# Kernel optimization log

Measured on AMD Instinct MI355X. Metric: run time of the kernel, lower is better.

## Reference

```python
import jax, jax.numpy as jnp
import numpy as np

D_MODEL = 1024
NUM_HEADS = 16
HEAD_DIM = D_MODEL // NUM_HEADS
B, S = 4, 2048


def _xavier(key, shape, gain=0.1):
    fan_in, fan_out = shape[1], shape[0]
    a = gain * np.sqrt(6.0 / (fan_in + fan_out))
    return jax.random.uniform(key, shape, jnp.float32, -a, a)


def setup_inputs() -> dict:
    key = jax.random.key(0)
    ks = jax.random.split(key, 11)
    inp = {
        "q": jax.random.normal(ks[0], (B, S, D_MODEL), jnp.float32),
        "k": jax.random.normal(ks[1], (B, S, D_MODEL), jnp.float32),
        "v": jax.random.normal(ks[2], (B, S, D_MODEL), jnp.float32),
        # nn.Linear weights are [out, in]; y = x @ W.T + b
        "Wq": _xavier(ks[3], (D_MODEL, D_MODEL)),
        "bq": jnp.zeros((D_MODEL,), jnp.float32),
        "Wk": _xavier(ks[4], (D_MODEL, D_MODEL)),
        "bk": jnp.zeros((D_MODEL,), jnp.float32),
        "Wv": _xavier(ks[5], (D_MODEL, D_MODEL)),
        "bv": jnp.zeros((D_MODEL,), jnp.float32),
        "Wo": _xavier(ks[6], (D_MODEL, D_MODEL)),
        "bo": jnp.zeros((D_MODEL,), jnp.float32),
    }
    return inp


def reference(q, k, v, Wq, bq, Wk, bk, Wv, bv, Wo, bo):
    b = q.shape[0]
    qh = (q @ Wq.T + bq).reshape(b, -1, NUM_HEADS, HEAD_DIM).transpose(0, 2, 1, 3)
    kh = (k @ Wk.T + bk).reshape(b, -1, NUM_HEADS, HEAD_DIM).transpose(0, 2, 1, 3)
    vh = (v @ Wv.T + bv).reshape(b, -1, NUM_HEADS, HEAD_DIM).transpose(0, 2, 1, 3)
    # NOTE: original (buggy) module scales by sqrt(d_model), not sqrt(head_dim)
    scale = 1.0 / jnp.sqrt(jnp.float32(D_MODEL))
    scores = jnp.einsum('bhqd,bhkd->bhqk', qh, kh) * scale  # [B,H,S,S]
    attn = jax.nn.softmax(scores, axis=-1)
    out = jnp.einsum('bhqk,bhkd->bhqd', attn, vh)
    out = out.transpose(0, 2, 1, 3).reshape(b, -1, D_MODEL)
    return out @ Wo.T + bo
```

## Files before the change

kernel.cpp:

```cpp
#include <hip/hip_runtime.h>

typedef unsigned short u16;
typedef short bf16x8 __attribute__((ext_vector_type(8)));
typedef float f32x4 __attribute__((ext_vector_type(4)));
typedef u16 u16x8 __attribute__((ext_vector_type(8)));

__device__ __forceinline__ u16 f2bf(float f) {
  unsigned u = __float_as_uint(f);
  u = u + 0x7fffu + ((u >> 16) & 1u);
  return (u16)(u >> 16);
}

__device__ __forceinline__ float fexp2(float x) {
#if __has_builtin(__builtin_amdgcn_exp2f)
  return __builtin_amdgcn_exp2f(x);
#else
  return exp2f(x);
#endif
}

#define GLD16(ldsp, gp)                                                         \
  __builtin_amdgcn_global_load_lds(                                             \
      (__attribute__((address_space(1))) void*)(void*)(gp),                     \
      (__attribute__((address_space(3))) void*)(ldsp), 16, 0, 0)

#define CVTPK(dst, lo, hi)                                                      \
  asm("v_cvt_pk_bf16_f32 %0, %1, %2" : "=v"(dst) : "v"(lo), "v"(hi))
#define PACK8(dst, a0, a1, a2, a3, a4, a5, a6, a7)                              \
  do {                                                                          \
    union { unsigned u_[4]; bf16x8 v_; } c_;                                    \
    CVTPK(c_.u_[0], a0, a1); CVTPK(c_.u_[1], a2, a3);                           \
    CVTPK(c_.u_[2], a4, a5); CVTPK(c_.u_[3], a6, a7);                           \
    dst = c_.v_;                                                                \
  } while (0)

__global__ __launch_bounds__(256) void pack_w4(const float* __restrict__ w0,
                                               const float* __restrict__ w1,
                                               const float* __restrict__ w2,
                                               const float* __restrict__ w3,
                                               u16* __restrict__ out) {
  int i = blockIdx.x * 256 + threadIdx.x;
  int which = i >> 17;
  const float* src = which == 0 ? w0 : which == 1 ? w1 : which == 2 ? w2 : w3;
  int j = i & 131071;
  const float4* p = (const float4*)src + (size_t)j * 2;
  float4 a = p[0], b = p[1];
  u16x8 r;
  r[0] = f2bf(a.x); r[1] = f2bf(a.y); r[2] = f2bf(a.z); r[3] = f2bf(a.w);
  r[4] = f2bf(b.x); r[5] = f2bf(b.y); r[6] = f2bf(b.z); r[7] = f2bf(b.w);
  *(u16x8*)(out + (size_t)i * 8) = r;
}

__global__ __launch_bounds__(256, 3)
void gemm_qkv(const float* __restrict__ qi, const float* __restrict__ ki,
              const float* __restrict__ vi, const u16* __restrict__ wbf,
              const float* __restrict__ bq, const float* __restrict__ bk,
              const float* __restrict__ bv, u16* __restrict__ qo,
              u16* __restrict__ ko, u16* __restrict__ vo) {
  constexpr int K = 1024;
  __shared__ __align__(16) u16 As[128 * 64];
  __shared__ __align__(16) u16 Bs[128 * 64];
  const int z = blockIdx.z;
  const float* Af = z == 0 ? qi : z == 1 ? ki : vi;
  const u16* Bw = wbf + ((size_t)z << 20);
  const float* bias = z == 0 ? bq : z == 1 ? bk : bv;

  const int t = threadIdx.x;
  const int w = t >> 6, l = t & 63;
  const int lr = l & 15, lg = l >> 4;
  const int flat = blockIdx.x | (blockIdx.y << 3);
  const int swz = ((flat & 7) << 6) | (flat >> 3);
  const int row0 = (swz >> 3) * 128, col0 = (swz & 7) * 128;
  const int wm = (w >> 1) * 64, wn = (w & 1) * 64;

  f32x4 acc[4][4] = {};

  const int ar = t >> 3;
  const int xw = ((t & 7) ^ (ar & 7)) * 16;
  const float* gA = Af + (size_t)(row0 + ar) * K + (t & 7) * 8;
  const u16* gB = Bw + (size_t)(col0 + ar) * K + (((t & 7) ^ (ar & 7)) * 8);
  u16* lB = &Bs[w * 512];

  float4 a0[4], a1[4];
#pragma unroll
  for (int j = 0; j < 4; ++j) {
    const float* p = gA + (size_t)j * 32 * K;
    a0[j] = *(const float4*)p;
    a1[j] = *(const float4*)(p + 4);
  }

  for (int kt = 0; kt < 16; ++kt) {
#pragma unroll
    for (int j = 0; j < 4; ++j)
      GLD16(lB + j * 2048, gB + (size_t)j * 32 * K + kt * 64);
#pragma unroll
    for (int j = 0; j < 4; ++j) {
      bf16x8 c;
      PACK8(c, a0[j].x, a0[j].y, a0[j].z, a0[j].w, a1[j].x, a1[j].y, a1[j].z, a1[j].w);
      *(bf16x8*)((char*)As + (ar + j * 32) * 128 + xw) = c;
    }
    __syncthreads();
    if (kt < 15) {
#pragma unroll
      for (int j = 0; j < 4; ++j) {
        const float* p = gA + (size_t)j * 32 * K + (kt + 1) * 64;
        a0[j] = *(const float4*)p;
        a1[j] = *(const float4*)(p + 4);
      }
    }
#pragma unroll
    for (int kh2 = 0; kh2 < 2; ++kh2) {
      bf16x8 aF[4], bF[4];
      const int bc = (kh2 * 64 + lg * 16) ^ ((lr & 7) * 16);
#pragma unroll
      for (int mi = 0; mi < 4; ++mi)
        aF[mi] = *(const bf16x8*)((const char*)As + (wm + mi * 16 + lr) * 128 + bc);
#pragma unroll
      for (int ni = 0; ni < 4; ++ni)
        bF[ni] = *(const bf16x8*)((const char*)Bs + (wn + ni * 16 + lr) * 128 + bc);
#pragma unroll
      for (int mi = 0; mi < 4; ++mi)
#pragma unroll
        for (int ni = 0; ni < 4; ++ni)
          acc[mi][ni] = __builtin_amdgcn_mfma_f32_16x16x32_bf16(aF[mi], bF[ni],
                                                                acc[mi][ni], 0, 0, 0);
    }
    __syncthreads();
  }

#pragma unroll
  for (int mi = 0; mi < 4; ++mi) {
#pragma unroll
    for (int ni = 0; ni < 4; ++ni) {
      const int n = col0 + wn + ni * 16 + lr;
      const float bvv = bias[n];
#pragma unroll
      for (int r = 0; r < 4; ++r) {
        const int m = row0 + wm + mi * 16 + lg * 4 + r;
        const float vv = acc[mi][ni][r] + bvv;
        const int bI = m >> 11, s = m & 2047, h = n >> 6, d = n & 63;
        if (z == 0) {
          qo[((size_t)((bI << 4) + h) * 2048 + s) * 64 + d] = f2bf(vv * 0.045084223f);
        } else if (z == 1) {
          ko[((size_t)((bI << 4) + h) * 2048 + s) * 64 + d] = f2bf(vv);
        } else {
          int bh = (bI << 4) + h, tile = s >> 6, kp = s & 63;
          int kM = kp >> 5, k5 = kp & 31;
          int kpp = kM * 32 + ((k5 >> 2) & 3) * 8 + (k5 >> 4) * 4 + (k5 & 3);
          int chunk = (kpp >> 3) ^ (d & 7);
          vo[((size_t)bh << 17) + tile * 4096 + d * 64 + chunk * 8 + (kpp & 7)] = f2bf(vv);
        }
      }
    }
  }
}

__global__ __launch_bounds__(256, 2)
void gemm_out(const u16* __restrict__ A, const u16* __restrict__ B,
              const float* __restrict__ bias, float* __restrict__ outp) {
  constexpr int K = 1024;
  __shared__ __align__(16) u16 As[128 * 64];
  __shared__ __align__(16) u16 Bs[128 * 64];
  const int t = threadIdx.x;
  const int w = t >> 6;
  const int l = t & 63;
  const int lr = l & 15, lg = l >> 4;
  const int flat = blockIdx.x | (blockIdx.y << 3);
  const int swz = ((flat & 7) << 6) | (flat >> 3);
  const int row0 = (swz >> 3) * 128, col0 = (swz & 7) * 128;
  const int wm = (w >> 1) * 64, wn = (w & 1) * 64;

  f32x4 acc[4][4] = {};

  const int srow = t >> 3;
  const int scol = ((t & 7) ^ (srow & 7)) * 8;
  const u16* gA = A + (size_t)(row0 + srow) * K + scol;
  const u16* gB = B + (size_t)(col0 + srow) * K + scol;
  u16* lA = &As[w * 512];
  u16* lB = &Bs[w * 512];

  for (int k0 = 0; k0 < K; k0 += 64) {
#pragma unroll
    for (int j = 0; j < 4; ++j) {
      GLD16(lA + j * 2048, gA + (size_t)j * 32 * K + k0);
      GLD16(lB + j * 2048, gB + (size_t)j * 32 * K + k0);
    }
    __syncthreads();
#pragma unroll
    for (int kh2 = 0; kh2 < 2; ++kh2) {
      bf16x8 aF[4], bF[4];
      const int bc = (kh2 * 64 + lg * 16) ^ ((lr & 7) * 16);
#pragma unroll
      for (int mi = 0; mi < 4; ++mi)
        aF[mi] = *(const bf16x8*)((const char*)As + (wm + mi * 16 + lr) * 128 + bc);
#pragma unroll
      for (int ni = 0; ni < 4; ++ni)
        bF[ni] = *(const bf16x8*)((const char*)Bs + (wn + ni * 16 + lr) * 128 + bc);
#pragma unroll
      for (int mi = 0; mi < 4; ++mi)
#pragma unroll
        for (int ni = 0; ni < 4; ++ni)
          acc[mi][ni] = __builtin_amdgcn_mfma_f32_16x16x32_bf16(aF[mi], bF[ni],
                                                                acc[mi][ni], 0, 0, 0);
    }
    __syncthreads();
  }

#pragma unroll
  for (int mi = 0; mi < 4; ++mi)
#pragma unroll
    for (int ni = 0; ni < 4; ++ni) {
      const int n = col0 + wn + ni * 16 + lr;
      const float bv = bias[n];
#pragma unroll
      for (int r = 0; r < 4; ++r) {
        const int m = row0 + wm + mi * 16 + lg * 4 + r;
        outp[(size_t)m * 1024 + n] = acc[mi][ni][r] + bv;
      }
    }
}

__global__ __launch_bounds__(256, 3)
void attn_fwd(const u16* __restrict__ qh, const u16* __restrict__ kh,
              const u16* __restrict__ vp, u16* __restrict__ aout) {
  __shared__ __align__(16) u16 Ks[2][4096];
  __shared__ __align__(16) u16 Vl[2][4096];
  const int t = threadIdx.x;
  const int w = t >> 6, l = t & 63;
  const int lr = l & 15, lg = l >> 4;
  const int flat = blockIdx.x | (blockIdx.y << 4);
  const int swz = ((flat & 7) << 7) | (flat >> 3);
  const int qb = swz & 15, bh = swz >> 4;
  const int q0 = qb * 128 + w * 32;

  bf16x8 qf[2][2];
#pragma unroll
  for (int qi = 0; qi < 2; ++qi) {
    const u16* qp = qh + ((size_t)bh * 2048 + q0 + qi * 16 + lr) * 64 + lg * 8;
    qf[qi][0] = *(const bf16x8*)qp;
    qf[qi][1] = *(const bf16x8*)(qp + 32);
  }

  f32x4 o0[4] = {}, o1[4] = {};
  f32x4 sm0 = {}, sm1 = {};
  const bf16x8 ones = {16256, 16256, 16256, 16256, 16256, 16256, 16256, 16256};

  const int krow = t >> 3, kseg = t & 7;
  const u16* gK = kh + ((size_t)bh * 2048 + krow) * 64 + ((kseg ^ (krow & 7)) * 8);
  const u16* gV = vp + ((size_t)bh << 17) + t * 8;

  const int xo0 = (lg * 16) ^ ((lr & 7) * 16);
  const int xo1 = xo0 ^ 64;

  {
    u16* kd = &Ks[0][0] + w * 512;
    u16* vd = &Vl[0][0] + w * 512;
    GLD16(kd, gK); GLD16(kd + 2048, gK + 2048);
    GLD16(vd, gV); GLD16(vd + 2048, gV + 2048);
    gK += 4096; gV += 4096;
  }
  __syncthreads();

  for (int tix = 0; tix < 32; ++tix) {
    const int cur = tix & 1;
    if (tix < 31) {
      u16* kd = &Ks[cur ^ 1][0] + w * 512;
      u16* vd = &Vl[cur ^ 1][0] + w * 512;
      GLD16(kd, gK); GLD16(kd + 2048, gK + 2048);
      GLD16(vd, gV); GLD16(vd + 2048, gV + 2048);
      gK += 4096; gV += 4096;
    }
    const char* kb = (const char*)&Ks[cur][0];
    f32x4 s0[4], s1[4];
    __builtin_amdgcn_s_setprio(1);
#pragma unroll
    for (int cq = 0; cq < 4; ++cq) {
      const char* rowp = kb + (cq * 16 + lr) * 128;
      bf16x8 kf0 = *(const bf16x8*)(rowp + xo0);
      bf16x8 kf1 = *(const bf16x8*)(rowp + xo1);
      f32x4 a = {}, b2 = {};
      a  = __builtin_amdgcn_mfma_f32_16x16x32_bf16(kf0, qf[0][0], a, 0, 0, 0);
      a  = __builtin_amdgcn_mfma_f32_16x16x32_bf16(kf1, qf[0][1], a, 0, 0, 0);
      b2 = __builtin_amdgcn_mfma_f32_16x16x32_bf16(kf0, qf[1][0], b2, 0, 0, 0);
      b2 = __builtin_amdgcn_mfma_f32_16x16x32_bf16(kf1, qf[1][1], b2, 0, 0, 0);
      s0[cq] = a; s1[cq] = b2;
    }
    __builtin_amdgcn_s_setprio(0);
    float p0[16], p1[16];
#pragma unroll
    for (int cq = 0; cq < 4; ++cq)
#pragma unroll
      for (int r = 0; r < 4; ++r) {
        p0[cq * 4 + r] = fexp2(s0[cq][r]);
        p1[cq * 4 + r] = fexp2(s1[cq][r]);
      }
    bf16x8 pA0, pA1, pB0, pB1;
    PACK8(pA0, p0[0], p0[1], p0[2], p0[3], p0[4], p0[5], p0[6], p0[7]);
    PACK8(pA1, p0[8], p0[9], p0[10], p0[11], p0[12], p0[13], p0[14], p0[15]);
    PACK8(pB0, p1[0], p1[1], p1[2], p1[3], p1[4], p1[5], p1[6], p1[7]);
    PACK8(pB1, p1[8], p1[9], p1[10], p1[11], p1[12], p1[13], p1[14], p1[15]);
    __builtin_amdgcn_s_setprio(1);
    sm0 = __builtin_amdgcn_mfma_f32_16x16x32_bf16(pA0, ones, sm0, 0, 0, 0);
    sm0 = __builtin_amdgcn_mfma_f32_16x16x32_bf16(pA1, ones, sm0, 0, 0, 0);
    sm1 = __builtin_amdgcn_mfma_f32_16x16x32_bf16(pB0, ones, sm1, 0, 0, 0);
    sm1 = __builtin_amdgcn_mfma_f32_16x16x32_bf16(pB1, ones, sm1, 0, 0, 0);
    const char* vbb = (const char*)&Vl[cur][0];
#pragma unroll
    for (int dc = 0; dc < 4; ++dc) {
      const char* rp = vbb + (dc * 16 + lr) * 128;
      bf16x8 vA = *(const bf16x8*)(rp + xo0);
      bf16x8 vB = *(const bf16x8*)(rp + xo1);
      o0[dc] = __builtin_amdgcn_mfma_f32_16x16x32_bf16(pA0, vA, o0[dc], 0, 0, 0);
      o0[dc] = __builtin_amdgcn_mfma_f32_16x16x32_bf16(pA1, vB, o0[dc], 0, 0, 0);
      o1[dc] = __builtin_amdgcn_mfma_f32_16x16x32_bf16(pB0, vA, o1[dc], 0, 0, 0);
      o1[dc] = __builtin_amdgcn_mfma_f32_16x16x32_bf16(pB1, vB, o1[dc], 0, 0, 0);
    }
    __builtin_amdgcn_s_setprio(0);
    __syncthreads();
  }

  const int b = bh >> 4, h = bh & 15;
#pragma unroll
  for (int r = 0; r < 4; ++r) {
    const float dA = 1.f / sm0[r];
    const float dB = 1.f / sm1[r];
    const size_t rowA = (size_t)b * 2048 + q0 + lg * 4 + r;
#pragma unroll
    for (int dc = 0; dc < 4; ++dc) {
      aout[rowA * 1024 + h * 64 + dc * 16 + lr] = f2bf(o0[dc][r] * dA);
      aout[(rowA + 16) * 1024 + h * 64 + dc * 16 + lr] = f2bf(o1[dc][r] * dB);
    }
  }
}

extern "C" void kernel_launch(void* const* d_in, const int* in_sizes, int n_in,
                              void* d_out, int out_size, void* d_ws, size_t ws_size,
                              hipStream_t stream) {
  const float* q  = (const float*)d_in[0];
  const float* k  = (const float*)d_in[1];
  const float* v  = (const float*)d_in[2];
  const float* Wq = (const float*)d_in[3];
  const float* bq = (const float*)d_in[4];
  const float* Wk = (const float*)d_in[5];
  const float* bk = (const float*)d_in[6];
  const float* Wv = (const float*)d_in[7];
  const float* bv = (const float*)d_in[8];
  const float* Wo = (const float*)d_in[9];
  const float* bo = (const float*)d_in[10];

  char* ws = (char*)d_ws;
  u16* wbf  = (u16*)(ws);
  u16* aout = (u16*)(ws + (8ull << 20));
  u16* qhB  = (u16*)(ws + (24ull << 20));
  u16* khB  = (u16*)(ws + (40ull << 20));
  u16* vtB  = (u16*)(ws + (56ull << 20));

  pack_w4<<<2048, 256, 0, stream>>>(Wq, Wk, Wv, Wo, wbf);
  gemm_qkv<<<dim3(8, 64, 3), 256, 0, stream>>>(q, k, v, wbf, bq, bk, bv,
                                               qhB, khB, vtB);
  attn_fwd<<<dim3(16, 64), 256, 0, stream>>>(qhB, khB, vtB, aout);
  gemm_out<<<dim3(8, 64), 256, 0, stream>>>(aout, wbf + (3u << 20), bo,
                                            (float*)d_out);

  (void)in_sizes; (void)n_in; (void)out_size; (void)ws_size;
}
```

Baseline: 171.2 us.

## Double-buffer LDS tiles in QKV and output projection GEMMs

```diff
diff --git a/kernel.cpp b/kernel.cpp
--- a/kernel.cpp
+++ b/kernel.cpp
@@ -59,7 +59,7 @@
               u16* __restrict__ ko, u16* __restrict__ vo) {
   constexpr int K = 1024;
   __shared__ __align__(16) u16 As[128 * 64];
-  __shared__ __align__(16) u16 Bs[128 * 64];
+  __shared__ __align__(16) u16 Bs[2][128 * 64];
   const int z = blockIdx.z;
   const float* Af = z == 0 ? qi : z == 1 ? ki : vi;
   const u16* Bw = wbf + ((size_t)z << 20);
@@ -79,7 +79,6 @@
   const int xw = ((t & 7) ^ (ar & 7)) * 16;
   const float* gA = Af + (size_t)(row0 + ar) * K + (t & 7) * 8;
   const u16* gB = Bw + (size_t)(col0 + ar) * K + (((t & 7) ^ (ar & 7)) * 8);
-  u16* lB = &Bs[w * 512];
 
   float4 a0[4], a1[4];
 #pragma unroll
@@ -88,19 +87,23 @@
     a0[j] = *(const float4*)p;
     a1[j] = *(const float4*)(p + 4);
   }
+#pragma unroll
+  for (int j = 0; j < 4; ++j)
+    GLD16(&Bs[0][w * 512] + j * 2048, gB + (size_t)j * 32 * K);
+#pragma unroll
+  for (int j = 0; j < 4; ++j) {
+    bf16x8 c;
+    PACK8(c, a0[j].x, a0[j].y, a0[j].z, a0[j].w, a1[j].x, a1[j].y, a1[j].z, a1[j].w);
+    *(bf16x8*)((char*)As + (ar + j * 32) * 128 + xw) = c;
+  }
+  __syncthreads();
 
   for (int kt = 0; kt < 16; ++kt) {
-#pragma unroll
-    for (int j = 0; j < 4; ++j)
-      GLD16(lB + j * 2048, gB + (size_t)j * 32 * K + kt * 64);
-#pragma unroll
-    for (int j = 0; j < 4; ++j) {
-      bf16x8 c;
-      PACK8(c, a0[j].x, a0[j].y, a0[j].z, a0[j].w, a1[j].x, a1[j].y, a1[j].z, a1[j].w);
-      *(bf16x8*)((char*)As + (ar + j * 32) * 128 + xw) = c;
-    }
-    __syncthreads();
+    const int cur = kt & 1;
     if (kt < 15) {
+#pragma unroll
+      for (int j = 0; j < 4; ++j)
+        GLD16(&Bs[cur ^ 1][w * 512] + j * 2048, gB + (size_t)j * 32 * K + (kt + 1) * 64);
 #pragma unroll
       for (int j = 0; j < 4; ++j) {
         const float* p = gA + (size_t)j * 32 * K + (kt + 1) * 64;
@@ -108,6 +111,7 @@
         a1[j] = *(const float4*)(p + 4);
       }
     }
+    const char* bsb = (const char*)&Bs[cur][0];
 #pragma unroll
     for (int kh2 = 0; kh2 < 2; ++kh2) {
       bf16x8 aF[4], bF[4];
@@ -117,7 +121,7 @@
         aF[mi] = *(const bf16x8*)((const char*)As + (wm + mi * 16 + lr) * 128 + bc);
 #pragma unroll
       for (int ni = 0; ni < 4; ++ni)
-        bF[ni] = *(const bf16x8*)((const char*)Bs + (wn + ni * 16 + lr) * 128 + bc);
+        bF[ni] = *(const bf16x8*)(bsb + (wn + ni * 16 + lr) * 128 + bc);
 #pragma unroll
       for (int mi = 0; mi < 4; ++mi)
 #pragma unroll
@@ -126,6 +130,15 @@
                                                                 acc[mi][ni], 0, 0, 0);
     }
     __syncthreads();
+    if (kt < 15) {
+#pragma unroll
+      for (int j = 0; j < 4; ++j) {
+        bf16x8 c;
+        PACK8(c, a0[j].x, a0[j].y, a0[j].z, a0[j].w, a1[j].x, a1[j].y, a1[j].z, a1[j].w);
+        *(bf16x8*)((char*)As + (ar + j * 32) * 128 + xw) = c;
+      }
+      __syncthreads();
+    }
   }
 
 #pragma unroll
@@ -159,8 +172,8 @@
 void gemm_out(const u16* __restrict__ A, const u16* __restrict__ B,
               const float* __restrict__ bias, float* __restrict__ outp) {
   constexpr int K = 1024;
-  __shared__ __align__(16) u16 As[128 * 64];
-  __shared__ __align__(16) u16 Bs[128 * 64];
+  __shared__ __align__(16) u16 As[2][128 * 64];
+  __shared__ __align__(16) u16 Bs[2][128 * 64];
   const int t = threadIdx.x;
   const int w = t >> 6;
   const int l = t & 63;
@@ -176,26 +189,35 @@
   const int scol = ((t & 7) ^ (srow & 7)) * 8;
   const u16* gA = A + (size_t)(row0 + srow) * K + scol;
   const u16* gB = B + (size_t)(col0 + srow) * K + scol;
-  u16* lA = &As[w * 512];
-  u16* lB = &Bs[w * 512];
-
-  for (int k0 = 0; k0 < K; k0 += 64) {
-#pragma unroll
-    for (int j = 0; j < 4; ++j) {
-      GLD16(lA + j * 2048, gA + (size_t)j * 32 * K + k0);
-      GLD16(lB + j * 2048, gB + (size_t)j * 32 * K + k0);
-    }
-    __syncthreads();
+
+#pragma unroll
+  for (int j = 0; j < 4; ++j) {
+    GLD16(&As[0][w * 512] + j * 2048, gA + (size_t)j * 32 * K);
+    GLD16(&Bs[0][w * 512] + j * 2048, gB + (size_t)j * 32 * K);
+  }
+  __syncthreads();
+
+  for (int kt = 0; kt < 16; ++kt) {
+    const int cur = kt & 1;
+    if (kt < 15) {
+#pragma unroll
+      for (int j = 0; j < 4; ++j) {
+        GLD16(&As[cur ^ 1][w * 512] + j * 2048, gA + (size_t)j * 32 * K + (kt + 1) * 64);
+        GLD16(&Bs[cur ^ 1][w * 512] + j * 2048, gB + (size_t)j * 32 * K + (kt + 1) * 64);
+      }
+    }
+    const char* asb = (const char*)&As[cur][0];
+    const char* bsb = (const char*)&Bs[cur][0];
 #pragma unroll
     for (int kh2 = 0; kh2 < 2; ++kh2) {
       bf16x8 aF[4], bF[4];
       const int bc = (kh2 * 64 + lg * 16) ^ ((lr & 7) * 16);
 #pragma unroll
       for (int mi = 0; mi < 4; ++mi)
-        aF[mi] = *(const bf16x8*)((const char*)As + (wm + mi * 16 + lr) * 128 + bc);
+        aF[mi] = *(const bf16x8*)(asb + (wm + mi * 16 + lr) * 128 + bc);
 #pragma unroll
       for (int ni = 0; ni < 4; ++ni)
-        bF[ni] = *(const bf16x8*)((const char*)Bs + (wn + ni * 16 + lr) * 128 + bc);
+        bF[ni] = *(const bf16x8*)(bsb + (wn + ni * 16 + lr) * 128 + bc);
 #pragma unroll
       for (int mi = 0; mi < 4; ++mi)
 #pragma unroll
```

Result: slower. 175.6 us (+2.5%).
